# Kernel tuning notes

Hardware: AMD Instinct MI355X
Metric: run time of the kernel (lower is better)

Reference implementation:

```python
import jax, jax.numpy as jnp
import numpy as np
import math

B, S, I, C = 1, 256, 512, 256   # batch, msa rows, residues, c_s
H, D = 8, 32                     # num_heads, head_dim; total = H*D = 256
EPS = 1e-5


def setup_inputs() -> dict:
    key = jax.random.key(0)
    ks = jax.random.split(key, 10)
    s = 0.02
    return {
        "msa_representation": jax.random.normal(ks[0], (B, S, I, C), jnp.float32),
        "ln_gamma": jnp.ones((C,), jnp.float32),
        "ln_beta": jnp.zeros((C,), jnp.float32),
        # weights stored [in, out] (torch Linear applies x @ W.T; equivalent math)
        "Wq": jax.random.normal(ks[1], (C, H * D), jnp.float32) * s,
        "Wk": jax.random.normal(ks[2], (C, D), jnp.float32) * s,
        "Wv": jax.random.normal(ks[3], (C, D), jnp.float32) * s,
        "Wg": jax.random.normal(ks[4], (C, H * D), jnp.float32) * s,
        "bg": jnp.zeros((H * D,), jnp.float32),
        "Wo": jax.random.normal(ks[5], (H * D, C), jnp.float32) * s,
        "bo": jnp.zeros((C,), jnp.float32),
    }


def reference(msa_representation, ln_gamma, ln_beta, Wq, Wk, Wv, Wg, bg, Wo, bo):
    x = msa_representation
    mu = jnp.mean(x, axis=-1, keepdims=True)
    var = jnp.mean(jnp.square(x - mu), axis=-1, keepdims=True)
    x = (x - mu) * jax.lax.rsqrt(var + EPS) * ln_gamma + ln_beta  # [B,S,I,C]

    Q = (x @ Wq).reshape(B, S, I, H, D).mean(axis=1)              # [B,I,H,D]
    K = x @ Wk                                                    # [B,S,I,D] ('btid')
    V = x @ Wv                                                    # [B,S,I,D]
    G = jax.nn.sigmoid(x @ Wg + bg).reshape(B, S, I, H, D)        # [B,S,I,H,D]

    scores = jnp.einsum('bihd,btid->bhti', Q, K) / math.sqrt(D)   # [B,H,S,I]
    attn = jax.nn.softmax(scores, axis=-2)                        # softmax over rows t
    weighted = jnp.einsum('bhti,btid->bihd', attn, V)             # [B,I,H,D]

    values = (G * weighted[:, None]).reshape(B, S, I, H * D)
    return values @ Wo + bo                                       # [B,S,I,C]
```

## Files before the change

### kernel.cpp

```cpp
#include <hip/hip_runtime.h>
#include <hip/hip_bf16.h>

#define S_DIM 256
#define I_DIM 512
#define NROWS (S_DIM * I_DIM)

using bf16x8 = __attribute__((ext_vector_type(8))) short;
using f32x4  = __attribute__((ext_vector_type(4))) float;
typedef unsigned short ushort_t;

__device__ __forceinline__ unsigned short f2bf(float f) {
  unsigned int u = __builtin_bit_cast(unsigned int, f);
  u += 0x7fffu + ((u >> 16) & 1u);
  return (unsigned short)(u >> 16);
}
__device__ __forceinline__ float bf2f(unsigned short u) {
  unsigned int x = ((unsigned int)u) << 16;
  return __builtin_bit_cast(float, x);
}
__device__ __forceinline__ void gl_lds16(const void* g, void* l) {
  __builtin_amdgcn_global_load_lds(
      (const __attribute__((address_space(1))) void*)g,
      (__attribute__((address_space(3))) void*)l, 16, 0, 0);
}

__global__ __launch_bounds__(256) void prep_weights(
    const float* __restrict__ Wk, const float* __restrict__ Wv,
    const float* __restrict__ Wg, const float* __restrict__ Wo,
    ushort_t* __restrict__ WkvT, ushort_t* __restrict__ WgT,
    ushort_t* __restrict__ WoT) {
  int t = blockIdx.x * 256 + threadIdx.x;
  int n = t >> 8, c = t & 255;
  if (t < 64 * 256) {
    float v = (n < 32) ? Wk[c * 32 + n] : Wv[c * 32 + (n - 32)];
    WkvT[t] = f2bf(v);
  }
  WgT[t] = f2bf(Wg[c * 256 + n]);
  WoT[t] = f2bf(Wo[c * 256 + n]);
}

__global__ __launch_bounds__(256) void ln_kernel(
    const float* __restrict__ x, const float* __restrict__ gamma,
    const float* __restrict__ beta, ushort_t* __restrict__ xn,
    float* __restrict__ xpart) {
  __shared__ float sacc[4][256];
  int b = blockIdx.x;
  int i = b & (I_DIM - 1);
  int sq = b >> 9;
  int w = threadIdx.x >> 6;
  int lane = threadIdx.x & 63;

  float4 gv = *(const float4*)(gamma + lane * 4);
  float4 bv = *(const float4*)(beta + lane * 4);
  float p0 = 0.f, p1 = 0.f, p2 = 0.f, p3 = 0.f;

#pragma unroll 4
  for (int it = 0; it < 16; ++it) {
    int s = sq * 64 + w * 16 + it;
    size_t row = (size_t)s * I_DIM + i;
    float4 xv = *(const float4*)(x + row * 256 + lane * 4);
    float sum = xv.x + xv.y + xv.z + xv.w;
    float sq2 = xv.x*xv.x + xv.y*xv.y + xv.z*xv.z + xv.w*xv.w;
#pragma unroll
    for (int off = 32; off >= 1; off >>= 1) {
      sum += __shfl_xor(sum, off);
      sq2 += __shfl_xor(sq2, off);
    }
    float mu = sum * (1.f / 256.f);
    float rs = rsqrtf(sq2 * (1.f / 256.f) - mu * mu + 1e-5f);
    float y0 = (xv.x - mu) * rs * gv.x + bv.x;
    float y1 = (xv.y - mu) * rs * gv.y + bv.y;
    float y2 = (xv.z - mu) * rs * gv.z + bv.z;
    float y3 = (xv.w - mu) * rs * gv.w + bv.w;
    ushort4 o;
    o.x = f2bf(y0); o.y = f2bf(y1); o.z = f2bf(y2); o.w = f2bf(y3);
    *(ushort4*)(xn + row * 256 + lane * 4) = o;
    p0 += y0; p1 += y1; p2 += y2; p3 += y3;
  }
  sacc[w][lane * 4 + 0] = p0;
  sacc[w][lane * 4 + 1] = p1;
  sacc[w][lane * 4 + 2] = p2;
  sacc[w][lane * 4 + 3] = p3;
  __syncthreads();
  int tid = threadIdx.x;
  xpart[((size_t)sq * I_DIM + i) * 256 + tid] =
      sacc[0][tid] + sacc[1][tid] + sacc[2][tid] + sacc[3][tid];
}

__global__ __launch_bounds__(256) void q_kernel(
    const float* __restrict__ xpart, const float* __restrict__ Wq,
    float* __restrict__ Q) {
  int i = blockIdx.x, col = threadIdx.x;
  __shared__ float xr[256];
  float s = xpart[((size_t)0 * I_DIM + i) * 256 + col]
          + xpart[((size_t)1 * I_DIM + i) * 256 + col]
          + xpart[((size_t)2 * I_DIM + i) * 256 + col]
          + xpart[((size_t)3 * I_DIM + i) * 256 + col];
  xr[col] = s * (1.f / 256.f);
  __syncthreads();
  float acc = 0.f;
#pragma unroll 8
  for (int c = 0; c < 256; ++c) acc = fmaf(xr[c], Wq[c * 256 + col], acc);
  Q[i * 256 + col] = acc * 0.17677669529663687f;
}

__global__ __launch_bounds__(256) void kv_kernel(
    const ushort_t* __restrict__ xn, const ushort_t* __restrict__ WkvT,
    ushort_t* __restrict__ KVb) {
  __shared__ __attribute__((aligned(16))) ushort_t xs[64 * 264];
  __shared__ __attribute__((aligned(16))) ushort_t wt[64 * 264];
  int tid = threadIdx.x;
  int m0 = blockIdx.x * 64;

  const uint4* xg = (const uint4*)(xn + (size_t)m0 * 256);
#pragma unroll
  for (int j = 0; j < 8; ++j) {
    int idx = tid + j * 256;
    *(uint4*)(&xs[(idx >> 5) * 264 + (idx & 31) * 8]) = xg[idx];
  }
  const uint4* wg_ = (const uint4*)WkvT;
#pragma unroll
  for (int j = 0; j < 8; ++j) {
    int idx = tid + j * 256;
    *(uint4*)(&wt[(idx >> 5) * 264 + (idx & 31) * 8]) = wg_[idx];
  }
  __syncthreads();

  int w = tid >> 6, lane = tid & 63;
  int m15 = lane & 15, q = lane >> 4;
  f32x4 acc[4] = {};
#pragma unroll
  for (int k = 0; k < 8; ++k) {
    bf16x8 a = *(const bf16x8*)(&xs[(w * 16 + m15) * 264 + k * 32 + q * 8]);
#pragma unroll
    for (int nt = 0; nt < 4; ++nt) {
      bf16x8 bb = *(const bf16x8*)(&wt[(nt * 16 + m15) * 264 + k * 32 + q * 8]);
      acc[nt] = __builtin_amdgcn_mfma_f32_16x16x32_bf16(a, bb, acc[nt], 0, 0, 0);
    }
  }
#pragma unroll
  for (int nt = 0; nt < 4; ++nt)
#pragma unroll
    for (int r = 0; r < 4; ++r)
      KVb[(size_t)(m0 + w * 16 + q * 4 + r) * 64 + nt * 16 + m15] = f2bf(acc[nt][r]);
}

__global__ __launch_bounds__(256) void attn_kernel(
    const ushort_t* __restrict__ KVb, const float* __restrict__ Q,
    float* __restrict__ weighted) {
  __shared__ ushort_t Vs[256 * 36];
  __shared__ float sl[8 * 264];
  __shared__ float ql[256];
  int i = blockIdx.x, tid = threadIdx.x;

  ql[tid] = Q[i * 256 + tid];
  const uint4* src = (const uint4*)(KVb + ((size_t)tid * I_DIM + i) * 64);
  uint4 kr0 = src[0], kr1 = src[1], kr2 = src[2], kr3 = src[3];
#pragma unroll
  for (int j = 0; j < 4; ++j) {
    uint4 v = src[4 + j];
    *(ushort4*)(&Vs[tid * 36 + j * 8 + 0]) = *(ushort4*)&v.x;
    *(ushort4*)(&Vs[tid * 36 + j * 8 + 4]) = *(ushort4*)&v.z;
  }
  ushort_t ks[32];
  *(uint4*)&ks[0] = kr0; *(uint4*)&ks[8] = kr1;
  *(uint4*)&ks[16] = kr2; *(uint4*)&ks[24] = kr3;
  float kf[32];
#pragma unroll
  for (int d = 0; d < 32; ++d) kf[d] = bf2f(ks[d]);
  __syncthreads();

#pragma unroll
  for (int h = 0; h < 8; ++h) {
    float sc = 0.f;
#pragma unroll
    for (int d = 0; d < 32; ++d) sc = fmaf(kf[d], ql[h * 32 + d], sc);
    sl[h * 264 + tid] = sc;
  }
  __syncthreads();

  int w = tid >> 6, lane = tid & 63;
#pragma unroll
  for (int hh = 0; hh < 2; ++hh) {
    int h = w * 2 + hh;
    float v0 = sl[h * 264 + lane], v1 = sl[h * 264 + lane + 64];
    float v2 = sl[h * 264 + lane + 128], v3 = sl[h * 264 + lane + 192];
    float m = fmaxf(fmaxf(v0, v1), fmaxf(v2, v3));
#pragma unroll
    for (int off = 32; off >= 1; off >>= 1) m = fmaxf(m, __shfl_xor(m, off));
    float e0 = __expf(v0 - m), e1 = __expf(v1 - m);
    float e2 = __expf(v2 - m), e3 = __expf(v3 - m);
    float ssum = e0 + e1 + e2 + e3;
#pragma unroll
    for (int off = 32; off >= 1; off >>= 1) ssum += __shfl_xor(ssum, off);
    float inv = 1.f / ssum;
    sl[h * 264 + lane] = e0 * inv;
    sl[h * 264 + lane + 64] = e1 * inv;
    sl[h * 264 + lane + 128] = e2 * inv;
    sl[h * 264 + lane + 192] = e3 * inv;
  }
  __syncthreads();

  int h = tid >> 5, d = tid & 31;
  float acc = 0.f;
#pragma unroll 4
  for (int t = 0; t < 256; ++t)
    acc = fmaf(sl[h * 264 + t], bf2f(Vs[t * 36 + d]), acc);
  weighted[i * 256 + tid] = acc;
}

__global__ __launch_bounds__(512) void fused_out_kernel(
    const ushort_t* __restrict__ xn, const ushort_t* __restrict__ WgT,
    const ushort_t* __restrict__ WoT, const float* __restrict__ weighted,
    const float* __restrict__ bg, const float* __restrict__ bo,
    float* __restrict__ out) {
  __shared__ __attribute__((aligned(16))) ushort_t xA[128 * 64];
  __shared__ __attribute__((aligned(16))) ushort_t Bs[256 * 64];
  __shared__ __attribute__((aligned(16))) ushort_t valS[128 * 256];
  const int tid = threadIdx.x;
  const int m0 = blockIdx.x * 128;
  const int w = tid >> 6, lane = tid & 63;
  const int m15 = lane & 15, q = lane >> 4;
  const int r2 = w >> 2, c4 = w & 3;

  f32x4 acc[4][4];
  const f32x4 zero = {0.f, 0.f, 0.f, 0.f};
#pragma unroll
  for (int t = 0; t < 4; ++t)
#pragma unroll
    for (int nt = 0; nt < 4; ++nt) acc[t][nt] = zero;

#pragma unroll 1
  for (int kc = 0; kc < 4; ++kc) {
    __syncthreads();
#pragma unroll
    for (int it = 0; it < 2; ++it) {
      int L = it * 512 + tid;
      int r = L >> 3, u = (L & 7) ^ (r & 7);
      gl_lds16(xn + (size_t)(m0 + r) * 256 + kc * 64 + u * 8,
               &xA[(it * 512 + w * 64) * 8]);
    }
#pragma unroll
    for (int it = 0; it < 4; ++it) {
      int L = it * 512 + tid;
      int n = L >> 3, u = (L & 7) ^ (n & 7);
      gl_lds16(WgT + (size_t)n * 256 + kc * 64 + u * 8,
               &Bs[(it * 512 + w * 64) * 8]);
    }
    __syncthreads();
#pragma unroll
    for (int kk = 0; kk < 2; ++kk) {
      bf16x8 bf[4], af[4];
#pragma unroll
      for (int nt = 0; nt < 4; ++nt) {
        int n = c4 * 64 + nt * 16 + m15;
        bf[nt] = *(const bf16x8*)&Bs[n * 64 + (((kk * 4 + q) ^ (n & 7)) * 8)];
      }
#pragma unroll
      for (int t = 0; t < 4; ++t) {
        int m = r2 * 64 + t * 16 + m15;
        af[t] = *(const bf16x8*)&xA[m * 64 + (((kk * 4 + q) ^ (m & 7)) * 8)];
      }
#pragma unroll
      for (int t = 0; t < 4; ++t)
#pragma unroll
        for (int nt = 0; nt < 4; ++nt)
          acc[t][nt] = __builtin_amdgcn_mfma_f32_16x16x32_bf16(af[t], bf[nt], acc[t][nt], 0, 0, 0);
    }
  }

#pragma unroll
  for (int nt = 0; nt < 4; ++nt) {
    int col = c4 * 64 + nt * 16 + m15;
    float bgi = bg[col];
#pragma unroll
    for (int t = 0; t < 4; ++t)
#pragma unroll
      for (int r = 0; r < 4; ++r) {
        int row = r2 * 64 + t * 16 + q * 4 + r;
        float pre = acc[t][nt][r] + bgi;
        float g = 1.f / (1.f + __expf(-pre));
        float vv = g * weighted[(size_t)((m0 + row) & (I_DIM - 1)) * 256 + col];
        valS[row * 256 + (((col >> 3) ^ (row & 7)) * 8) + (col & 7)] = f2bf(vv);
      }
  }
#pragma unroll
  for (int t = 0; t < 4; ++t)
#pragma unroll
    for (int nt = 0; nt < 4; ++nt) acc[t][nt] = zero;

#pragma unroll 1
  for (int kc = 0; kc < 4; ++kc) {
    __syncthreads();
#pragma unroll
    for (int it = 0; it < 4; ++it) {
      int L = it * 512 + tid;
      int n = L >> 3, u = (L & 7) ^ (n & 7);
      gl_lds16(WoT + (size_t)n * 256 + kc * 64 + u * 8,
               &Bs[(it * 512 + w * 64) * 8]);
    }
    __syncthreads();
#pragma unroll
    for (int kk = 0; kk < 2; ++kk) {
      bf16x8 bf[4], af[4];
#pragma unroll
      for (int nt = 0; nt < 4; ++nt) {
        int n = c4 * 64 + nt * 16 + m15;
        bf[nt] = *(const bf16x8*)&Bs[n * 64 + (((kk * 4 + q) ^ (n & 7)) * 8)];
      }
#pragma unroll
      for (int t = 0; t < 4; ++t) {
        int m = r2 * 64 + t * 16 + m15;
        int u = kc * 8 + kk * 4 + q;
        af[t] = *(const bf16x8*)&valS[m * 256 + ((u ^ (m & 7)) * 8)];
      }
#pragma unroll
      for (int t = 0; t < 4; ++t)
#pragma unroll
        for (int nt = 0; nt < 4; ++nt)
          acc[t][nt] = __builtin_amdgcn_mfma_f32_16x16x32_bf16(af[t], bf[nt], acc[t][nt], 0, 0, 0);
    }
  }

#pragma unroll
  for (int nt = 0; nt < 4; ++nt) {
    int col = c4 * 64 + nt * 16 + m15;
    float boi = bo[col];
#pragma unroll
    for (int t = 0; t < 4; ++t)
#pragma unroll
      for (int r = 0; r < 4; ++r) {
        int row = r2 * 64 + t * 16 + q * 4 + r;
        out[(size_t)(m0 + row) * 256 + col] = acc[t][nt][r] + boi;
      }
  }
}

extern "C" void kernel_launch(void* const* d_in, const int* in_sizes, int n_in,
                              void* d_out, int out_size, void* d_ws, size_t ws_size,
                              hipStream_t stream) {
  const float* msa = (const float*)d_in[0];
  const float* gam = (const float*)d_in[1];
  const float* bet = (const float*)d_in[2];
  const float* Wq  = (const float*)d_in[3];
  const float* Wk  = (const float*)d_in[4];
  const float* Wv  = (const float*)d_in[5];
  const float* Wg  = (const float*)d_in[6];
  const float* bg  = (const float*)d_in[7];
  const float* Wo  = (const float*)d_in[8];
  const float* bo  = (const float*)d_in[9];
  float* out = (float*)d_out;

  char* ws = (char*)d_ws;
  ushort_t* xn     = (ushort_t*)ws;
  float* xpart     = (float*)(ws + 67108864);
  float* Q         = (float*)(ws + 69206016);
  ushort_t* KVb    = (ushort_t*)(ws + 69730304);
  float* weighted  = (float*)(ws + 86507520);
  ushort_t* WkvT   = (ushort_t*)(ws + 87031808);
  ushort_t* WgT    = (ushort_t*)(ws + 87064576);
  ushort_t* WoT    = (ushort_t*)(ws + 87195648);

  prep_weights<<<256, 256, 0, stream>>>(Wk, Wv, Wg, Wo, WkvT, WgT, WoT);
  ln_kernel<<<2048, 256, 0, stream>>>(msa, gam, bet, xn, xpart);
  q_kernel<<<512, 256, 0, stream>>>(xpart, Wq, Q);
  kv_kernel<<<2048, 256, 0, stream>>>(xn, WkvT, KVb);
  attn_kernel<<<512, 256, 0, stream>>>(KVb, Q, weighted);
  fused_out_kernel<<<1024, 512, 0, stream>>>(xn, WgT, WoT, weighted, bg, bo, out);
}
```

Baseline: 382.5 us.

## Split fused gate/output GEMM into two kernels to cut LDS usage

The fused gate+output kernel becomes two kernels. The first computes the sigmoid gate times the attention output and writes the bf16 values in place over the normalized activations buffer. The second reads them back for the Wo projection. This removes the 64KB valS shared buffer, lowering LDS per block from about 112KB to 48KB so more blocks can be resident. The cost is an extra 64MB global write and read of the intermediate plus one more launch.

```diff
diff --git a/kernel.cpp b/kernel.cpp
--- a/kernel.cpp
+++ b/kernel.cpp
@@ -209,14 +209,12 @@
   weighted[i * 256 + tid] = acc;
 }
 
-__global__ __launch_bounds__(512) void fused_out_kernel(
-    const ushort_t* __restrict__ xn, const ushort_t* __restrict__ WgT,
-    const ushort_t* __restrict__ WoT, const float* __restrict__ weighted,
-    const float* __restrict__ bg, const float* __restrict__ bo,
-    float* __restrict__ out) {
-  __shared__ __attribute__((aligned(16))) ushort_t xA[128 * 64];
+__global__ __launch_bounds__(512) void gate_val_kernel(
+    ushort_t* xv,
+    const ushort_t* __restrict__ WgT, const float* __restrict__ weighted,
+    const float* __restrict__ bg) {
+  __shared__ __attribute__((aligned(16))) ushort_t As[128 * 64];
   __shared__ __attribute__((aligned(16))) ushort_t Bs[256 * 64];
-  __shared__ __attribute__((aligned(16))) ushort_t valS[128 * 256];
   const int tid = threadIdx.x;
   const int m0 = blockIdx.x * 128;
   const int w = tid >> 6, lane = tid & 63;
@@ -237,8 +235,8 @@
     for (int it = 0; it < 2; ++it) {
       int L = it * 512 + tid;
       int r = L >> 3, u = (L & 7) ^ (r & 7);
-      gl_lds16(xn + (size_t)(m0 + r) * 256 + kc * 64 + u * 8,
-               &xA[(it * 512 + w * 64) * 8]);
+      gl_lds16(xv + (size_t)(m0 + r) * 256 + kc * 64 + u * 8,
+               &As[(it * 512 + w * 64) * 8]);
     }
 #pragma unroll
     for (int it = 0; it < 4; ++it) {
@@ -259,7 +257,7 @@
 #pragma unroll
       for (int t = 0; t < 4; ++t) {
         int m = r2 * 64 + t * 16 + m15;
-        af[t] = *(const bf16x8*)&xA[m * 64 + (((kk * 4 + q) ^ (m & 7)) * 8)];
+        af[t] = *(const bf16x8*)&As[m * 64 + (((kk * 4 + q) ^ (m & 7)) * 8)];
       }
 #pragma unroll
       for (int t = 0; t < 4; ++t)
@@ -281,9 +279,24 @@
         float pre = acc[t][nt][r] + bgi;
         float g = 1.f / (1.f + __expf(-pre));
         float vv = g * weighted[(size_t)((m0 + row) & (I_DIM - 1)) * 256 + col];
-        valS[row * 256 + (((col >> 3) ^ (row & 7)) * 8) + (col & 7)] = f2bf(vv);
-      }
-  }
+        xv[(size_t)(m0 + row) * 256 + col] = f2bf(vv);
+      }
+  }
+}
+
+__global__ __launch_bounds__(512) void out_kernel(
+    const ushort_t* __restrict__ val, const ushort_t* __restrict__ WoT,
+    const float* __restrict__ bo, float* __restrict__ out) {
+  __shared__ __attribute__((aligned(16))) ushort_t As[128 * 64];
+  __shared__ __attribute__((aligned(16))) ushort_t Bs[256 * 64];
+  const int tid = threadIdx.x;
+  const int m0 = blockIdx.x * 128;
+  const int w = tid >> 6, lane = tid & 63;
+  const int m15 = lane & 15, q = lane >> 4;
+  const int r2 = w >> 2, c4 = w & 3;
+
+  f32x4 acc[4][4];
+  const f32x4 zero = {0.f, 0.f, 0.f, 0.f};
 #pragma unroll
   for (int t = 0; t < 4; ++t)
 #pragma unroll
@@ -292,6 +305,13 @@
 #pragma unroll 1
   for (int kc = 0; kc < 4; ++kc) {
     __syncthreads();
+#pragma unroll
+    for (int it = 0; it < 2; ++it) {
+      int L = it * 512 + tid;
+      int r = L >> 3, u = (L & 7) ^ (r & 7);
+      gl_lds16(val + (size_t)(m0 + r) * 256 + kc * 64 + u * 8,
+               &As[(it * 512 + w * 64) * 8]);
+    }
 #pragma unroll
     for (int it = 0; it < 4; ++it) {
       int L = it * 512 + tid;
@@ -311,8 +331,7 @@
 #pragma unroll
       for (int t = 0; t < 4; ++t) {
         int m = r2 * 64 + t * 16 + m15;
-        int u = kc * 8 + kk * 4 + q;
-        af[t] = *(const bf16x8*)&valS[m * 256 + ((u ^ (m & 7)) * 8)];
+        af[t] = *(const bf16x8*)&As[m * 64 + (((kk * 4 + q) ^ (m & 7)) * 8)];
       }
 #pragma unroll
       for (int t = 0; t < 4; ++t)
@@ -366,5 +385,6 @@
   q_kernel<<<512, 256, 0, stream>>>(xpart, Wq, Q);
   kv_kernel<<<2048, 256, 0, stream>>>(xn, WkvT, KVb);
   attn_kernel<<<512, 256, 0, stream>>>(KVb, Q, weighted);
-  fused_out_kernel<<<1024, 512, 0, stream>>>(xn, WgT, WoT, weighted, bg, bo, out);
-}
+  gate_val_kernel<<<1024, 512, 0, stream>>>(xn, WgT, weighted, bg);
+  out_kernel<<<1024, 512, 0, stream>>>(xn, WoT, bo, out);
+}
```

Result: slower. 392.9 us (+2.7%).
